# Optimization experiments

Hardware: AMD Instinct MI355X
Metric: run time of the kernel (lower is better)

The kernel has to match this reference:

```python
import jax, jax.numpy as jnp
import numpy as np

# Dims: N tokens, D input, H expert hidden, O output, E experts, G gate hidden, K top-k
N, D, H, O, E, G, K = 8192, 1024, 2048, 1024, 8, 256, 2
BALANCE_COEF = 0.01


def setup_inputs() -> dict:
    key = jax.random.key(0)
    ks = jax.random.split(key, 12)
    def lin(k, shape, fan_in):
        return jax.random.normal(k, shape, jnp.float32) * (1.0 / np.sqrt(fan_in))
    return {
        "x":   jax.random.normal(ks[0], (N, D), jnp.float32),
        # gating MLP: D -> G -> E
        "Wg1": lin(ks[1], (D, G), D), "bg1": jnp.zeros((G,), jnp.float32),
        "Wg2": lin(ks[2], (G, E), G), "bg2": jnp.zeros((E,), jnp.float32),
        # stacked expert MLPs: D -> H -> H -> O (ExpertNetwork, num_layers=2)
        "W1": lin(ks[3], (E, D, H), D), "b1": jnp.zeros((E, H), jnp.float32),
        "W2": lin(ks[4], (E, H, H), H), "b2": jnp.zeros((E, H), jnp.float32),
        "W3": lin(ks[5], (E, H, O), H), "b3": jnp.zeros((E, O), jnp.float32),
    }


def reference(x, Wg1, bg1, Wg2, bg2, W1, b1, W2, b2, W3, b3):
    # Gating: 2-layer MLP -> softmax -> top-k -> renormalize (eval: no noise/dropout)
    logits = jnp.maximum(x @ Wg1 + bg1, 0.0) @ Wg2 + bg2            # [N, E]
    probs = jax.nn.softmax(logits, axis=-1)
    w, idx = jax.lax.top_k(probs, K)                                # [N, K]
    w = w / jnp.sum(w, axis=-1, keepdims=True)
    onehot = jax.nn.one_hot(idx, E, dtype=x.dtype)                  # [N, K, E]
    comb = jnp.sum(onehot * w[..., None], axis=1)                   # [N, E] per-token expert weight

    # Dense-equivalent combine: unselected tokens get weight 0, identical math to
    # the masked dispatch + scatter-add in the torch code.
    def expert_step(acc, params):
        W1e, b1e, W2e, b2e, W3e, b3e, we = params                   # we: [N]
        h = jnp.maximum(x @ W1e + b1e, 0.0)                         # [N, H]
        h = jnp.maximum(h @ W2e + b2e, 0.0)                         # [N, H]
        o = h @ W3e + b3e                                           # [N, O]
        return acc + o * we[:, None], None

    out, _ = jax.lax.scan(expert_step, jnp.zeros((N, O), x.dtype),
                          (W1, b1, W2, b2, W3, b3, comb.T))

    # aux losses: expert_usage[e] = sum_i mean_b(indices[b,i]==e)
    expert_usage = jnp.sum(onehot, axis=(0, 1)) / N                 # [E]
    balance_loss = jnp.mean((expert_usage - 1.0 / E) ** 2) * BALANCE_COEF
    return out, balance_loss, expert_usage
```

## Files before the change

### kernel.cpp

```cpp
#include <hip/hip_runtime.h>
#include <hip/hip_bf16.h>
#include <cstdint>
#include <cstddef>

#define N_TOK 8192
#define D_IN  1024
#define H_DIM 2048
#define O_DIM 1024
#define E_NUM 8
#define G_DIM 256
#define MAXTILES 136
#define MAXROWS  (MAXTILES*128)

typedef __attribute__((ext_vector_type(8))) __bf16 bf16x8;
typedef __attribute__((ext_vector_type(4))) __bf16 bf16x4;
typedef __attribute__((ext_vector_type(4))) float floatx4;

#define GCAST(p) ((__attribute__((address_space(1))) void*)(void*)(p))
#define LCAST(p) ((__attribute__((address_space(3))) void*)(p))

__global__ __launch_bounds__(256) void cast_x_kernel(const float* __restrict__ x,
                                                     __bf16* __restrict__ xb) {
  int i = (blockIdx.x * 256 + threadIdx.x) * 4;
  float4 v = *reinterpret_cast<const float4*>(x + i);
  bf16x4 o;
  o.x = (__bf16)v.x; o.y = (__bf16)v.y; o.z = (__bf16)v.z; o.w = (__bf16)v.w;
  *reinterpret_cast<bf16x4*>(xb + i) = o;
}

__global__ __launch_bounds__(256) void transpose_w_kernel(const float* __restrict__ src,
                                                          __bf16* __restrict__ dst,
                                                          int K, int N) {
  __shared__ float tl[64][68];
  int e = blockIdx.z;
  const float* s = src + (size_t)e * K * N;
  __bf16* d = dst + (size_t)e * K * N;
  int k0 = blockIdx.y * 64, n0 = blockIdx.x * 64;
  int t = threadIdx.x;
  int kr = t >> 4, nc = t & 15;
#pragma unroll
  for (int p = 0; p < 4; p++) {
    float4 v = *reinterpret_cast<const float4*>(
        s + (size_t)(k0 + kr + p * 16) * N + n0 + nc * 4);
    *reinterpret_cast<float4*>(&tl[kr + p * 16][nc * 4]) = v;
  }
  __syncthreads();
  int n = t >> 2, kg = t & 3;
#pragma unroll
  for (int p = 0; p < 2; p++) {
    bf16x8 o;
#pragma unroll
    for (int j = 0; j < 8; j++) o[j] = (__bf16)tl[p * 32 + kg * 8 + j][n];
    *reinterpret_cast<bf16x8*>(d + (size_t)(n0 + n) * K + k0 + p * 32 + kg * 8) = o;
  }
}

__global__ __launch_bounds__(256) void gate1_kernel(const float* __restrict__ x,
                                                    const float* __restrict__ Wg1,
                                                    const float* __restrict__ bg1,
                                                    float* __restrict__ g) {
  __shared__ float As[32][68];
  __shared__ float Bs[32][68];
  int bn = blockIdx.x, bm = blockIdx.y;
  int t = threadIdx.x;
  int tm = t >> 4, tn = t & 15;
  float acc[4][4] = {};
  for (int k0 = 0; k0 < D_IN; k0 += 32) {
#pragma unroll
    for (int i = 0; i < 2; i++) {
      int idx = t + 256 * i;
      int row = idx >> 3, c4 = idx & 7;
      float4 v = *reinterpret_cast<const float4*>(
          x + (size_t)(bm * 64 + row) * D_IN + k0 + c4 * 4);
      As[c4 * 4 + 0][row] = v.x;
      As[c4 * 4 + 1][row] = v.y;
      As[c4 * 4 + 2][row] = v.z;
      As[c4 * 4 + 3][row] = v.w;
      int brow = idx >> 4, bc4 = idx & 15;
      float4 wv = *reinterpret_cast<const float4*>(
          Wg1 + (size_t)(k0 + brow) * G_DIM + bn * 64 + bc4 * 4);
      *reinterpret_cast<float4*>(&Bs[brow][bc4 * 4]) = wv;
    }
    __syncthreads();
#pragma unroll
    for (int k = 0; k < 32; k++) {
      float4 av = *reinterpret_cast<const float4*>(&As[k][tm * 4]);
      float4 bv = *reinterpret_cast<const float4*>(&Bs[k][tn * 4]);
      float a4[4] = {av.x, av.y, av.z, av.w};
      float b4[4] = {bv.x, bv.y, bv.z, bv.w};
#pragma unroll
      for (int r = 0; r < 4; r++)
#pragma unroll
        for (int c = 0; c < 4; c++) acc[r][c] = fmaf(a4[r], b4[c], acc[r][c]);
    }
    __syncthreads();
  }
  int gr = bm * 64 + tm * 4, gc = bn * 64 + tn * 4;
#pragma unroll
  for (int r = 0; r < 4; r++) {
    float4 o;
    o.x = fmaxf(acc[r][0] + bg1[gc + 0], 0.f);
    o.y = fmaxf(acc[r][1] + bg1[gc + 1], 0.f);
    o.z = fmaxf(acc[r][2] + bg1[gc + 2], 0.f);
    o.w = fmaxf(acc[r][3] + bg1[gc + 3], 0.f);
    *reinterpret_cast<float4*>(g + (size_t)(gr + r) * G_DIM + gc) = o;
  }
}

__global__ __launch_bounds__(256) void gate2_kernel(const float* __restrict__ g,
                                                    const float* __restrict__ Wg2,
                                                    const float* __restrict__ bg2,
                                                    int* __restrict__ top_idx,
                                                    float* __restrict__ top_w,
                                                    int* __restrict__ counts) {
  __shared__ float lg[32][9];
  int t = threadIdx.x;
  int tl = t >> 3, e = t & 7;
  int n = blockIdx.x * 32 + tl;
  const float* gr = g + (size_t)n * G_DIM;
  float acc = bg2[e];
  for (int i = 0; i < G_DIM; i += 4) {
    float4 v = *reinterpret_cast<const float4*>(gr + i);
    acc += v.x * Wg2[(i + 0) * E_NUM + e];
    acc += v.y * Wg2[(i + 1) * E_NUM + e];
    acc += v.z * Wg2[(i + 2) * E_NUM + e];
    acc += v.w * Wg2[(i + 3) * E_NUM + e];
  }
  lg[tl][e] = acc;
  __syncthreads();
  if (e == 0) {
    float l[8];
#pragma unroll
    for (int i = 0; i < 8; i++) l[i] = lg[tl][i];
    int i0 = 0;
    for (int i = 1; i < 8; i++)
      if (l[i] > l[i0]) i0 = i;
    int i1 = (i0 == 0) ? 1 : 0;
    for (int i = 0; i < 8; i++)
      if (i != i0 && l[i] > l[i1]) i1 = i;
    float d = expf(l[i1] - l[i0]);
    float w0 = 1.f / (1.f + d);
    float w1 = d * w0;
    top_idx[n * 2 + 0] = i0;
    top_idx[n * 2 + 1] = i1;
    top_w[n * 2 + 0] = w0;
    top_w[n * 2 + 1] = w1;
    atomicAdd(&counts[i0], 1);
    atomicAdd(&counts[i1], 1);
  }
}

__global__ void g3_kernel(const int* __restrict__ counts, int* __restrict__ cursors,
                          int* __restrict__ off_pad, int* __restrict__ ntiles,
                          int* __restrict__ tile_meta, float* __restrict__ out_tail,
                          int* __restrict__ slot_token, float* __restrict__ slot_w) {
  if (threadIdx.x == 0) {
    int off = 0, nt = 0;
    float mse = 0.f;
    for (int e = 0; e < E_NUM; e++) {
      off_pad[e] = off;
      int c = counts[e];
      int tiles = (c + 127) >> 7;
      for (int i = 0; i < tiles; i++) {
        tile_meta[nt * 2 + 0] = e;
        tile_meta[nt * 2 + 1] = off + i * 128;
        nt++;
      }
      off += tiles << 7;
      cursors[e] = 0;
      float u = (float)c / (float)N_TOK;
      out_tail[1 + e] = u;
      float dd = u - 0.125f;
      mse += dd * dd;
    }
    *ntiles = nt;
    out_tail[0] = (mse / 8.0f) * 0.01f;
  }
  for (int s = threadIdx.x; s < MAXROWS; s += 256) {
    slot_token[s] = 0;
    slot_w[s] = 0.f;
  }
}

__global__ __launch_bounds__(256) void scatter_kernel(const int* __restrict__ top_idx,
                                                      const float* __restrict__ top_w,
                                                      const int* __restrict__ off_pad,
                                                      int* __restrict__ cursors,
                                                      int* __restrict__ slot_token,
                                                      float* __restrict__ slot_w) {
  int n = blockIdx.x * 256 + threadIdx.x;
#pragma unroll
  for (int k = 0; k < 2; k++) {
    int e = top_idx[n * 2 + k];
    int pos = atomicAdd(&cursors[e], 1);
    int s = off_pad[e] + pos;
    slot_token[s] = n;
    slot_w[s] = top_w[n * 2 + k];
  }
}

__global__ __launch_bounds__(256) void moe_gemm_kernel(
    const __bf16* __restrict__ A, int Astride, int gatherA,
    const __bf16* __restrict__ Wt, const float* __restrict__ bias,
    int Kdim, int Ndim,
    const int* __restrict__ tile_meta, const int* __restrict__ ntiles_p,
    const int* __restrict__ slot_token, const float* __restrict__ slot_w,
    __bf16* __restrict__ h_out, float* __restrict__ out_final, int finalMode) {
  int tile = blockIdx.y;
  if (tile >= *ntiles_p) return;
  __shared__ __bf16 As[128 * 32];
  __shared__ __bf16 Bs[128 * 32];
  int ex = tile_meta[tile * 2 + 0];
  int slot0 = tile_meta[tile * 2 + 1];
  int n0 = blockIdx.x * 128;
  int t = threadIdx.x, l = t & 63, w = t >> 6;

  size_t aoff[2], boff[2];
#pragma unroll
  for (int i = 0; i < 2; i++) {
    int gidx = (w * 2 + i) * 64 + l;
    int row = gidx >> 2;
    int kch = (gidx & 3) ^ ((row >> 1) & 3);
    int sl = slot0 + row;
    long long rb = gatherA ? (long long)slot_token[sl] * Astride
                           : (long long)sl * Astride;
    aoff[i] = (size_t)rb + kch * 8;
    boff[i] = ((size_t)ex * Ndim + n0 + row) * (size_t)Kdim + kch * 8;
  }

  int wm = (w >> 1) * 64, wn = (w & 1) * 64;
  int lm = l & 15, lq = l >> 4;
  floatx4 acc[4][4] = {};

  for (int k0 = 0; k0 < Kdim; k0 += 32) {
#pragma unroll
    for (int i = 0; i < 2; i++) {
      __builtin_amdgcn_global_load_lds(GCAST(A + aoff[i] + k0),
                                       LCAST((char*)As + w * 2048 + i * 1024),
                                       16, 0, 0);
      __builtin_amdgcn_global_load_lds(GCAST(Wt + boff[i] + k0),
                                       LCAST((char*)Bs + w * 2048 + i * 1024),
                                       16, 0, 0);
    }
    __syncthreads();
    bf16x8 af[4], bfr[4];
#pragma unroll
    for (int i = 0; i < 4; i++) {
      int r = wm + i * 16 + lm;
      int s = lq ^ ((r >> 1) & 3);
      af[i] = *reinterpret_cast<const bf16x8*>(As + r * 32 + s * 8);
    }
#pragma unroll
    for (int j = 0; j < 4; j++) {
      int r = wn + j * 16 + lm;
      int s = lq ^ ((r >> 1) & 3);
      bfr[j] = *reinterpret_cast<const bf16x8*>(Bs + r * 32 + s * 8);
    }
#pragma unroll
    for (int i = 0; i < 4; i++)
#pragma unroll
      for (int j = 0; j < 4; j++)
        acc[i][j] = __builtin_amdgcn_mfma_f32_16x16x32_bf16(af[i], bfr[j], acc[i][j], 0, 0, 0);
    __syncthreads();
  }

  float bcol[4];
#pragma unroll
  for (int j = 0; j < 4; j++) bcol[j] = bias[(size_t)ex * Ndim + n0 + wn + j * 16 + lm];

  if (finalMode) {
#pragma unroll
    for (int i = 0; i < 4; i++) {
#pragma unroll
      for (int r = 0; r < 4; r++) {
        int sl = slot0 + wm + i * 16 + lq * 4 + r;
        int tok = slot_token[sl];
        float wgt = slot_w[sl];
        if (wgt != 0.f) {
          float* orow = out_final + (size_t)tok * Ndim + n0 + wn + lm;
#pragma unroll
          for (int j = 0; j < 4; j++) {
            float v = acc[i][j][r] + bcol[j];
            atomicAdd(orow + j * 16, wgt * v);
          }
        }
      }
    }
  } else {
#pragma unroll
    for (int i = 0; i < 4; i++) {
#pragma unroll
      for (int r = 0; r < 4; r++) {
        int sl = slot0 + wm + i * 16 + lq * 4 + r;
        __bf16* hrow = h_out + (size_t)sl * Ndim + n0 + wn + lm;
#pragma unroll
        for (int j = 0; j < 4; j++) {
          float v = fmaxf(acc[i][j][r] + bcol[j], 0.f);
          hrow[j * 16] = (__bf16)v;
        }
      }
    }
  }
}

extern "C" void kernel_launch(void* const* d_in, const int* in_sizes, int n_in,
                              void* d_out, int out_size, void* d_ws, size_t ws_size,
                              hipStream_t stream) {
  const float* x   = (const float*)d_in[0];
  const float* Wg1 = (const float*)d_in[1];
  const float* bg1 = (const float*)d_in[2];
  const float* Wg2 = (const float*)d_in[3];
  const float* bg2 = (const float*)d_in[4];
  const float* W1  = (const float*)d_in[5];
  const float* b1  = (const float*)d_in[6];
  const float* W2  = (const float*)d_in[7];
  const float* b2  = (const float*)d_in[8];
  const float* W3  = (const float*)d_in[9];
  const float* b3  = (const float*)d_in[10];
  float* out = (float*)d_out;

  char* ws = (char*)d_ws;
  __bf16* x_bf       = (__bf16*)(ws + 0);
  __bf16* W1t        = (__bf16*)(ws + 16777216);
  __bf16* W2t        = (__bf16*)(ws + 50331648);
  __bf16* W3t        = (__bf16*)(ws + 117440512);
  __bf16* h1         = (__bf16*)(ws + 150994944);
  __bf16* h2         = (__bf16*)(ws + 222298112);
  float*  gbuf       = (float*) (ws + 293601280);
  int*    top_idx    = (int*)   (ws + 301989888);
  float*  top_w      = (float*) (ws + 302055424);
  int*    slot_token = (int*)   (ws + 302120960);
  float*  slot_w     = (float*) (ws + 302190592);
  int*    meta       = (int*)   (ws + 302260224);
  int* counts    = meta;
  int* cursors   = meta + 8;
  int* off_pad   = meta + 16;
  int* ntiles    = meta + 24;
  int* tile_meta = meta + 32;
  float* out_tail = out + (size_t)N_TOK * O_DIM;

  hipMemsetAsync(d_out, 0, ((size_t)N_TOK * O_DIM + 9) * sizeof(float), stream);
  hipMemsetAsync(meta, 0, 64, stream);

  cast_x_kernel<<<(N_TOK * D_IN) / 1024, 256, 0, stream>>>(x, x_bf);
  transpose_w_kernel<<<dim3(H_DIM / 64, D_IN / 64, E_NUM), 256, 0, stream>>>(W1, W1t, D_IN, H_DIM);
  transpose_w_kernel<<<dim3(H_DIM / 64, H_DIM / 64, E_NUM), 256, 0, stream>>>(W2, W2t, H_DIM, H_DIM);
  transpose_w_kernel<<<dim3(O_DIM / 64, H_DIM / 64, E_NUM), 256, 0, stream>>>(W3, W3t, H_DIM, O_DIM);

  gate1_kernel<<<dim3(G_DIM / 64, N_TOK / 64), 256, 0, stream>>>(x, Wg1, bg1, gbuf);
  gate2_kernel<<<N_TOK / 32, 256, 0, stream>>>(gbuf, Wg2, bg2, top_idx, top_w, counts);
  g3_kernel<<<1, 256, 0, stream>>>(counts, cursors, off_pad, ntiles, tile_meta, out_tail,
                                   slot_token, slot_w);
  scatter_kernel<<<N_TOK / 256, 256, 0, stream>>>(top_idx, top_w, off_pad, cursors,
                                                  slot_token, slot_w);

  moe_gemm_kernel<<<dim3(H_DIM / 128, MAXTILES), 256, 0, stream>>>(
      x_bf, D_IN, 1, W1t, b1, D_IN, H_DIM, tile_meta, ntiles, slot_token, slot_w,
      h1, nullptr, 0);
  moe_gemm_kernel<<<dim3(H_DIM / 128, MAXTILES), 256, 0, stream>>>(
      h1, H_DIM, 0, W2t, b2, H_DIM, H_DIM, tile_meta, ntiles, slot_token, slot_w,
      h2, nullptr, 0);
  moe_gemm_kernel<<<dim3(O_DIM / 128, MAXTILES), 256, 0, stream>>>(
      h2, H_DIM, 0, W3t, b3, H_DIM, O_DIM, tile_meta, ntiles, slot_token, slot_w,
      nullptr, out, 1);
}
```

Measured before the change: 1.095 ms.

## Merge prep kernels into one launch and replace atomic scatter with slot-indexed combine

Merges the x cast, gate layer-1 GEMM and the three weight-transpose kernels into one prep kernel that picks its job from the block index. The final expert GEMM now writes per-slot outputs to a buffer that reuses the h1 region, and a new combine kernel gathers each token's two slots and applies the gate weights. This drops the output memset and the float atomicAdds into the output, at the cost of an extra write and read of the per-slot output buffer. Padded slots point to token 0, which is harmless here because only real slots are read back.

```diff
diff --git a/kernel.cpp b/kernel.cpp
--- a/kernel.cpp
+++ b/kernel.cpp
@@ -19,23 +19,20 @@
 #define GCAST(p) ((__attribute__((address_space(1))) void*)(void*)(p))
 #define LCAST(p) ((__attribute__((address_space(3))) void*)(p))
 
-__global__ __launch_bounds__(256) void cast_x_kernel(const float* __restrict__ x,
-                                                     __bf16* __restrict__ xb) {
-  int i = (blockIdx.x * 256 + threadIdx.x) * 4;
-  float4 v = *reinterpret_cast<const float4*>(x + i);
-  bf16x4 o;
-  o.x = (__bf16)v.x; o.y = (__bf16)v.y; o.z = (__bf16)v.z; o.w = (__bf16)v.w;
-  *reinterpret_cast<bf16x4*>(xb + i) = o;
-}
-
-__global__ __launch_bounds__(256) void transpose_w_kernel(const float* __restrict__ src,
-                                                          __bf16* __restrict__ dst,
-                                                          int K, int N) {
-  __shared__ float tl[64][68];
-  int e = blockIdx.z;
+#define JOB_G1_END   512
+#define JOB_CAST_END 4608
+#define JOB_W1_END   8704
+#define JOB_W2_END   16896
+#define JOB_W3_END   20992
+
+__device__ inline void transpose_body(const float* __restrict__ src,
+                                      __bf16* __restrict__ dst,
+                                      int K, int N, int e, int ktile, int ntile,
+                                      float* smemf) {
+  float (*tl)[68] = (float(*)[68])smemf;
   const float* s = src + (size_t)e * K * N;
   __bf16* d = dst + (size_t)e * K * N;
-  int k0 = blockIdx.y * 64, n0 = blockIdx.x * 64;
+  int k0 = ktile * 64, n0 = ntile * 64;
   int t = threadIdx.x;
   int kr = t >> 4, nc = t & 15;
 #pragma unroll
@@ -55,13 +52,13 @@
   }
 }
 
-__global__ __launch_bounds__(256) void gate1_kernel(const float* __restrict__ x,
-                                                    const float* __restrict__ Wg1,
-                                                    const float* __restrict__ bg1,
-                                                    float* __restrict__ g) {
-  __shared__ float As[32][68];
-  __shared__ float Bs[32][68];
-  int bn = blockIdx.x, bm = blockIdx.y;
+__device__ inline void gate1_body(const float* __restrict__ x,
+                                  const float* __restrict__ Wg1,
+                                  const float* __restrict__ bg1,
+                                  float* __restrict__ g,
+                                  int bn, int bm, float* smemf) {
+  float (*As)[68] = (float(*)[68])smemf;
+  float (*Bs)[68] = (float(*)[68])(smemf + 32 * 68);
   int t = threadIdx.x;
   int tm = t >> 4, tn = t & 15;
   float acc[4][4] = {};
@@ -104,6 +101,38 @@
     o.z = fmaxf(acc[r][2] + bg1[gc + 2], 0.f);
     o.w = fmaxf(acc[r][3] + bg1[gc + 3], 0.f);
     *reinterpret_cast<float4*>(g + (size_t)(gr + r) * G_DIM + gc) = o;
+  }
+}
+
+__global__ __launch_bounds__(256) void prep_kernel(
+    const float* __restrict__ x, __bf16* __restrict__ xb,
+    const float* __restrict__ W1, __bf16* __restrict__ W1t,
+    const float* __restrict__ W2, __bf16* __restrict__ W2t,
+    const float* __restrict__ W3, __bf16* __restrict__ W3t,
+    const float* __restrict__ Wg1, const float* __restrict__ bg1,
+    float* __restrict__ g) {
+  __shared__ float smemf[4352];
+  int b = blockIdx.x;
+  if (b < JOB_G1_END) {
+    gate1_body(x, Wg1, bg1, g, b & 3, b >> 2, smemf);
+  } else if (b < JOB_CAST_END) {
+    int id = b - JOB_G1_END;
+    int i = id * 2048 + threadIdx.x * 8;
+    float4 v0 = *reinterpret_cast<const float4*>(x + i);
+    float4 v1 = *reinterpret_cast<const float4*>(x + i + 4);
+    bf16x8 o;
+    o[0] = (__bf16)v0.x; o[1] = (__bf16)v0.y; o[2] = (__bf16)v0.z; o[3] = (__bf16)v0.w;
+    o[4] = (__bf16)v1.x; o[5] = (__bf16)v1.y; o[6] = (__bf16)v1.z; o[7] = (__bf16)v1.w;
+    *reinterpret_cast<bf16x8*>(xb + i) = o;
+  } else if (b < JOB_W1_END) {
+    int id = b - JOB_CAST_END;
+    transpose_body(W1, W1t, D_IN, H_DIM, id >> 9, (id >> 5) & 15, id & 31, smemf);
+  } else if (b < JOB_W2_END) {
+    int id = b - JOB_W1_END;
+    transpose_body(W2, W2t, H_DIM, H_DIM, id >> 10, (id >> 5) & 31, id & 31, smemf);
+  } else {
+    int id = b - JOB_W2_END;
+    transpose_body(W3, W3t, H_DIM, O_DIM, id >> 9, (id >> 4) & 31, id & 15, smemf);
   }
 }
 
@@ -153,7 +182,7 @@
 __global__ void g3_kernel(const int* __restrict__ counts, int* __restrict__ cursors,
                           int* __restrict__ off_pad, int* __restrict__ ntiles,
                           int* __restrict__ tile_meta, float* __restrict__ out_tail,
-                          int* __restrict__ slot_token, float* __restrict__ slot_w) {
+                          int* __restrict__ slot_token) {
   if (threadIdx.x == 0) {
     int off = 0, nt = 0;
     float mse = 0.f;
@@ -176,18 +205,14 @@
     *ntiles = nt;
     out_tail[0] = (mse / 8.0f) * 0.01f;
   }
-  for (int s = threadIdx.x; s < MAXROWS; s += 256) {
-    slot_token[s] = 0;
-    slot_w[s] = 0.f;
-  }
+  for (int s = threadIdx.x; s < MAXROWS; s += 256) slot_token[s] = 0;
 }
 
 __global__ __launch_bounds__(256) void scatter_kernel(const int* __restrict__ top_idx,
-                                                      const float* __restrict__ top_w,
                                                       const int* __restrict__ off_pad,
                                                       int* __restrict__ cursors,
                                                       int* __restrict__ slot_token,
-                                                      float* __restrict__ slot_w) {
+                                                      int* __restrict__ token_slots) {
   int n = blockIdx.x * 256 + threadIdx.x;
 #pragma unroll
   for (int k = 0; k < 2; k++) {
@@ -195,7 +220,7 @@
     int pos = atomicAdd(&cursors[e], 1);
     int s = off_pad[e] + pos;
     slot_token[s] = n;
-    slot_w[s] = top_w[n * 2 + k];
+    token_slots[n * 2 + k] = s;
   }
 }
 
@@ -204,8 +229,8 @@
     const __bf16* __restrict__ Wt, const float* __restrict__ bias,
     int Kdim, int Ndim,
     const int* __restrict__ tile_meta, const int* __restrict__ ntiles_p,
-    const int* __restrict__ slot_token, const float* __restrict__ slot_w,
-    __bf16* __restrict__ h_out, float* __restrict__ out_final, int finalMode) {
+    const int* __restrict__ slot_token,
+    __bf16* __restrict__ h_out, float* __restrict__ y_out, int finalMode) {
   int tile = blockIdx.y;
   if (tile >= *ntiles_p) return;
   __shared__ __bf16 As[128 * 32];
@@ -274,16 +299,9 @@
 #pragma unroll
       for (int r = 0; r < 4; r++) {
         int sl = slot0 + wm + i * 16 + lq * 4 + r;
-        int tok = slot_token[sl];
-        float wgt = slot_w[sl];
-        if (wgt != 0.f) {
-          float* orow = out_final + (size_t)tok * Ndim + n0 + wn + lm;
-#pragma unroll
-          for (int j = 0; j < 4; j++) {
-            float v = acc[i][j][r] + bcol[j];
-            atomicAdd(orow + j * 16, wgt * v);
-          }
-        }
+        float* yrow = y_out + (size_t)sl * Ndim + n0 + wn + lm;
+#pragma unroll
+        for (int j = 0; j < 4; j++) yrow[j * 16] = acc[i][j][r] + bcol[j];
       }
     }
   } else {
@@ -301,6 +319,24 @@
       }
     }
   }
+}
+
+__global__ __launch_bounds__(256) void combine_kernel(const float* __restrict__ y,
+                                                      const int* __restrict__ token_slots,
+                                                      const float* __restrict__ top_w,
+                                                      float* __restrict__ out) {
+  int n = blockIdx.x;
+  int t = threadIdx.x;
+  int s0 = token_slots[n * 2 + 0], s1 = token_slots[n * 2 + 1];
+  float w0 = top_w[n * 2 + 0], w1 = top_w[n * 2 + 1];
+  float4 a = reinterpret_cast<const float4*>(y + (size_t)s0 * O_DIM)[t];
+  float4 b = reinterpret_cast<const float4*>(y + (size_t)s1 * O_DIM)[t];
+  float4 o;
+  o.x = w0 * a.x + w1 * b.x;
+  o.y = w0 * a.y + w1 * b.y;
+  o.z = w0 * a.z + w1 * b.z;
+  o.w = w0 * a.w + w1 * b.w;
+  reinterpret_cast<float4*>(out + (size_t)n * O_DIM)[t] = o;
 }
 
 extern "C" void kernel_launch(void* const* d_in, const int* in_sizes, int n_in,
@@ -326,11 +362,12 @@
   __bf16* W3t        = (__bf16*)(ws + 117440512);
   __bf16* h1         = (__bf16*)(ws + 150994944);
   __bf16* h2         = (__bf16*)(ws + 222298112);
+  float*  y          = (float*) (ws + 150994944);
   float*  gbuf       = (float*) (ws + 293601280);
   int*    top_idx    = (int*)   (ws + 301989888);
   float*  top_w      = (float*) (ws + 302055424);
   int*    slot_token = (int*)   (ws + 302120960);
-  float*  slot_w     = (float*) (ws + 302190592);
+  int*    token_slots= (int*)   (ws + 302190592);
   int*    meta       = (int*)   (ws + 302260224);
   int* counts    = meta;
   int* cursors   = meta + 8;
@@ -339,28 +376,24 @@
   int* tile_meta = meta + 32;
   float* out_tail = out + (size_t)N_TOK * O_DIM;
 
-  hipMemsetAsync(d_out, 0, ((size_t)N_TOK * O_DIM + 9) * sizeof(float), stream);
   hipMemsetAsync(meta, 0, 64, stream);
 
-  cast_x_kernel<<<(N_TOK * D_IN) / 1024, 256, 0, stream>>>(x, x_bf);
-  transpose_w_kernel<<<dim3(H_DIM / 64, D_IN / 64, E_NUM), 256, 0, stream>>>(W1, W1t, D_IN, H_DIM);
-  transpose_w_kernel<<<dim3(H_DIM / 64, H_DIM / 64, E_NUM), 256, 0, stream>>>(W2, W2t, H_DIM, H_DIM);
-  transpose_w_kernel<<<dim3(O_DIM / 64, H_DIM / 64, E_NUM), 256, 0, stream>>>(W3, W3t, H_DIM, O_DIM);
-
-  gate1_kernel<<<dim3(G_DIM / 64, N_TOK / 64), 256, 0, stream>>>(x, Wg1, bg1, gbuf);
+  prep_kernel<<<JOB_W3_END, 256, 0, stream>>>(x, x_bf, W1, W1t, W2, W2t, W3, W3t,
+                                              Wg1, bg1, gbuf);
   gate2_kernel<<<N_TOK / 32, 256, 0, stream>>>(gbuf, Wg2, bg2, top_idx, top_w, counts);
   g3_kernel<<<1, 256, 0, stream>>>(counts, cursors, off_pad, ntiles, tile_meta, out_tail,
-                                   slot_token, slot_w);
-  scatter_kernel<<<N_TOK / 256, 256, 0, stream>>>(top_idx, top_w, off_pad, cursors,
-                                                  slot_token, slot_w);
+                                   slot_token);
+  scatter_kernel<<<N_TOK / 256, 256, 0, stream>>>(top_idx, off_pad, cursors,
+                                                  slot_token, token_slots);
 
   moe_gemm_kernel<<<dim3(H_DIM / 128, MAXTILES), 256, 0, stream>>>(
-      x_bf, D_IN, 1, W1t, b1, D_IN, H_DIM, tile_meta, ntiles, slot_token, slot_w,
+      x_bf, D_IN, 1, W1t, b1, D_IN, H_DIM, tile_meta, ntiles, slot_token,
       h1, nullptr, 0);
   moe_gemm_kernel<<<dim3(H_DIM / 128, MAXTILES), 256, 0, stream>>>(
-      h1, H_DIM, 0, W2t, b2, H_DIM, H_DIM, tile_meta, ntiles, slot_token, slot_w,
+      h1, H_DIM, 0, W2t, b2, H_DIM, H_DIM, tile_meta, ntiles, slot_token,
       h2, nullptr, 0);
   moe_gemm_kernel<<<dim3(O_DIM / 128, MAXTILES), 256, 0, stream>>>(
-      h2, H_DIM, 0, W3t, b3, H_DIM, O_DIM, tile_meta, ntiles, slot_token, slot_w,
-      nullptr, out, 1);
-}
+      h2, H_DIM, 0, W3t, b3, H_DIM, O_DIM, tile_meta, ntiles, slot_token,
+      nullptr, y, 1);
+  combine_kernel<<<N_TOK, 256, 0, stream>>>(y, token_slots, top_w, out);
+}
```

After: 1.051 ms. 1.04x faster.
